# Optimization experiments

Hardware: AMD Instinct MI355X
Metric: run time of the kernel (lower is better)

Reference implementation:

```python
import jax, jax.numpy as jnp
import numpy as np

BAND_WIDTH = 0.05
EPS = 1e-5
NORM_EPS = 1e-12  # F.normalize clamp_min


def _l2_normalize_channels(x):
    # x: (B, C, D, H, W); normalize over channel dim=1 like F.normalize(p=2, dim=1)
    n = jnp.sqrt(jnp.sum(x * x, axis=1, keepdims=True))
    return x / jnp.maximum(n, NORM_EPS)


def setup_inputs() -> dict:
    key = jax.random.key(0)
    k1, k2, k3 = jax.random.split(key, 3)
    B, C, D, H, W = 2, 256, 8, 8, 8
    P, K = 128, 512  # n_patches iterations, k=512 sampled voxels per patch
    S = D * H * W  # 512 spatial voxels
    t2_feat = jax.random.normal(k1, (B, C, D, H, W), dtype=jnp.float32)
    t1_feat = jax.random.normal(k2, (B, C, D, H, W), dtype=jnp.float32)
    idx = jax.random.randint(k3, (P, K), 0, S, dtype=jnp.int32)
    return {"t2_feat": t2_feat, "t1_feat": t1_feat, "idx": idx}


def reference(t2_feat, t1_feat, idx):
    B, C = t2_feat.shape[:2]
    # normalize channels, flatten spatial dims: (B, C, S)
    t2 = _l2_normalize_channels(t2_feat).reshape(B, C, -1)
    t1 = _l2_normalize_channels(t1_feat).reshape(B, C, -1)
    # gather the same random voxels for both modalities: (B, C, P, K)
    t2p = t2[:, :, idx]
    t1p = t1[:, :, idx]
    # batched cosine similarity: bmm(t2p^T, t1p) per patch -> (P, B, K, K)
    cs = jnp.einsum('bcpk,bcpl->pbkl', t2p, t1p)
    e = jnp.exp(cs / BAND_WIDTH)
    pos = jnp.diagonal(e, axis1=2, axis2=3)  # (P, B, K) exp of positives
    # InfoNCE over columns (torch dim=1 of (B,K,K)) and rows (dim=2)
    info_nce1 = pos / jnp.sum(e, axis=2)
    info_nce2 = pos / jnp.sum(e, axis=3)
    info_nce = 0.5 * (info_nce1 + info_nce2)
    # per-patch mean of -log, then mean over patches == global mean
    return jnp.mean(-jnp.log(info_nce + EPS))
```

## Files before the change

### kernel.cpp

```cpp
#include <hip/hip_runtime.h>

typedef __attribute__((ext_vector_type(8))) short bf16x8;
typedef __attribute__((ext_vector_type(4))) float f32x4;

#define C_DIM 256
#define S_DIM 512
#define P_DIM 128
#define K_DIM 512
#define INV_BW 20.0f
#define EPS_LOSS 1e-5f

#define OFF_P2PART 0
#define OFF_P1PART 16384
#define OFF_DIAG   32768
#define OFF_CNTBF  33792
#define OFF_EBF    66560
#define OFF_ETBF   328704
#define OFF_D1P    590848
#define OFF_D2P    852992
#define OFF_PART   1115136
#define OFF_TICKET 1115264

__device__ inline ushort f2bf(float f) {
  union { float f; uint u; } v; v.f = f;
  return (ushort)((v.u + 0x7FFF + ((v.u >> 16) & 1)) >> 16);
}

__global__ __launch_bounds__(512) void pre_kernel(
    const float* __restrict__ t2, const float* __restrict__ t1,
    const int* __restrict__ idx,
    float* __restrict__ p2part, float* __restrict__ p1part,
    ushort* __restrict__ cntbf, int* __restrict__ ticket) {
  int blk = blockIdx.x, t = threadIdx.x;
  if (blk < 32) {
    int b = blk >> 4, g = blk & 15;
    const float* p2 = t2 + b * (C_DIM * S_DIM) + (g * 16) * S_DIM + t;
    const float* p1 = t1 + b * (C_DIM * S_DIM) + (g * 16) * S_DIM + t;
    float a2 = 0.f, a1 = 0.f;
    #pragma unroll
    for (int c = 0; c < 16; ++c) {
      float v2 = p2[c * S_DIM]; a2 += v2 * v2;
      float v1 = p1[c * S_DIM]; a1 += v1 * v1;
    }
    p2part[(b * 16 + g) * S_DIM + t] = a2;
    p1part[(b * 16 + g) * S_DIM + t] = a1;
  } else {
    __shared__ int c_lds[S_DIM];
    int p = blk - 32;
    if (blk == 32 && t == 0) *ticket = 0;
    c_lds[t] = 0;
    __syncthreads();
    atomicAdd(&c_lds[idx[p * K_DIM + t]], 1);
    __syncthreads();
    cntbf[p * S_DIM + t] = f2bf((float)c_lds[t]);
  }
}

__global__ __launch_bounds__(256) void gemm_exp_kernel(
    const float* __restrict__ t2, const float* __restrict__ t1,
    const float* __restrict__ p2part, const float* __restrict__ p1part,
    ushort* __restrict__ Ebf, ushort* __restrict__ ETbf,
    float* __restrict__ diag) {
  __shared__ float At[128][32];
  __shared__ float Bt[128][32];
  __shared__ float As[32], Bs[32];
  int b  = blockIdx.z;
  int s0 = blockIdx.y * 32;
  int t0 = blockIdx.x * 32;
  int tid = threadIdx.x;
  if (tid < 64) {
    int lane = tid & 31;
    const float* src = (tid < 32) ? p2part : p1part;
    int col = ((tid < 32) ? s0 : t0) + lane;
    float ss = 0.f;
    #pragma unroll
    for (int j = 0; j < 16; ++j) ss += src[(b * 16 + j) * S_DIM + col];
    float sc = 1.0f / fmaxf(sqrtf(ss), 1e-12f);
    if (tid < 32) As[lane] = sc; else Bs[lane] = sc;
  }
  __syncthreads();
  int sl = tid & 31, cr = tid >> 5;
  int tx = tid & 15, ty = tid >> 4;
  float ascale = As[sl], bscale = Bs[sl];
  const float* base2 = t2 + b * (C_DIM * S_DIM);
  const float* base1 = t1 + b * (C_DIM * S_DIM);
  float acc00 = 0.f, acc01 = 0.f, acc10 = 0.f, acc11 = 0.f;
  for (int cc = 0; cc < 2; ++cc) {
    int c0 = cc * 128;
    #pragma unroll
    for (int i = 0; i < 16; ++i) {
      int c = cr * 16 + i;
      At[c][sl] = base2[(c0 + c) * S_DIM + s0 + sl] * ascale;
      Bt[c][sl] = base1[(c0 + c) * S_DIM + t0 + sl] * bscale;
    }
    __syncthreads();
    #pragma unroll 8
    for (int c = 0; c < 128; ++c) {
      float2 a  = *reinterpret_cast<const float2*>(&At[c][tx * 2]);
      float2 bv = *reinterpret_cast<const float2*>(&Bt[c][ty * 2]);
      acc00 += a.x * bv.x; acc01 += a.x * bv.y;
      acc10 += a.y * bv.x; acc11 += a.y * bv.y;
    }
    __syncthreads();
  }
  int r0 = s0 + tx * 2, c0o = t0 + ty * 2;
  float e00 = expf(acc00 * INV_BW), e01 = expf(acc01 * INV_BW);
  float e10 = expf(acc10 * INV_BW), e11 = expf(acc11 * INV_BW);
  ushort* Eb  = Ebf  + b * (S_DIM * S_DIM);
  ushort* ETb = ETbf + b * (S_DIM * S_DIM);
  *reinterpret_cast<uint*>(&Eb[r0 * S_DIM + c0o]) =
      (uint)f2bf(e00) | ((uint)f2bf(e01) << 16);
  *reinterpret_cast<uint*>(&Eb[(r0 + 1) * S_DIM + c0o]) =
      (uint)f2bf(e10) | ((uint)f2bf(e11) << 16);
  *reinterpret_cast<uint*>(&ETb[c0o * S_DIM + r0]) =
      (uint)f2bf(e00) | ((uint)f2bf(e10) << 16);
  *reinterpret_cast<uint*>(&ETb[(c0o + 1) * S_DIM + r0]) =
      (uint)f2bf(e01) | ((uint)f2bf(e11) << 16);
  if (blockIdx.x == blockIdx.y && tx == ty) {
    diag[b * S_DIM + r0]     = e00;
    diag[b * S_DIM + r0 + 1] = e11;
  }
}

__global__ __launch_bounds__(256) void denom_mfma_kernel(
    const ushort* __restrict__ Ebf, const ushort* __restrict__ ETbf,
    const ushort* __restrict__ cntbf,
    float* __restrict__ D1p, float* __restrict__ D2p) {
  int wave = threadIdx.x >> 6, lane = threadIdx.x & 63;
  int job = blockIdx.x * 4 + wave;
  int n = job & 31, m = (job >> 5) & 7, b = (job >> 8) & 1;
  int z = (job >> 9) & 1, h = job >> 10;
  int m0 = m * 16, col0 = n * 16;
  const ushort* Bmat = (z ? Ebf : ETbf) + b * (S_DIM * S_DIM);
  float* Dp = (z ? D2p : D1p) + h * (P_DIM * 2 * S_DIM);
  int lr = lane & 15, lo = lane >> 4;
  const ushort* aptr = cntbf + (m0 + lr) * S_DIM + h * 256 + lo * 8;
  const ushort* bptr = Bmat + (col0 + lr) * S_DIM + h * 256 + lo * 8;
  f32x4 acc = {0.f, 0.f, 0.f, 0.f};
  #pragma unroll
  for (int k = 0; k < 8; ++k) {
    bf16x8 af = *reinterpret_cast<const bf16x8*>(aptr + k * 32);
    bf16x8 bfv = *reinterpret_cast<const bf16x8*>(bptr + k * 32);
    acc = __builtin_amdgcn_mfma_f32_16x16x32_bf16(af, bfv, acc, 0, 0, 0);
  }
  #pragma unroll
  for (int r = 0; r < 4; ++r) {
    int p = m0 + lo * 4 + r;
    Dp[(p * 2 + b) * S_DIM + col0 + lr] = acc[r];
  }
}

__global__ __launch_bounds__(512) void loss_final_kernel(
    const int* __restrict__ idx, const float* __restrict__ diag,
    const float* __restrict__ D1p, const float* __restrict__ D2p,
    float* __restrict__ part, int* __restrict__ ticket, float* __restrict__ out) {
  const int HOFF = P_DIM * 2 * S_DIM;
  int p = blockIdx.x, k = threadIdx.x;
  int s = idx[p * K_DIM + k];
  float acc = 0.f;
  #pragma unroll
  for (int b = 0; b < 2; ++b) {
    float pos = diag[b * S_DIM + s];
    int o = (p * 2 + b) * S_DIM + s;
    float d1 = D1p[o] + D1p[HOFF + o];
    float d2 = D2p[o] + D2p[HOFF + o];
    acc += logf(0.5f * (pos / d1 + pos / d2) + EPS_LOSS);
  }
  for (int o = 32; o; o >>= 1) acc += __shfl_down(acc, o);
  __shared__ float red[8];
  __shared__ int lastflag;
  if ((k & 63) == 0) red[k >> 6] = acc;
  __syncthreads();
  if (k == 0) {
    float tsum = 0.f;
    #pragma unroll
    for (int i = 0; i < 8; ++i) tsum += red[i];
    atomicExch(&part[p], tsum);
    __threadfence();
    int old = atomicAdd(ticket, 1);
    lastflag = (old == P_DIM - 1);
  }
  __syncthreads();
  if (lastflag) {
    __threadfence();
    float v = (k < P_DIM) ? atomicAdd(&part[k], 0.0f) : 0.0f;
    for (int o = 32; o; o >>= 1) v += __shfl_down(v, o);
    __shared__ float red2[8];
    if ((k & 63) == 0) red2[k >> 6] = v;
    __syncthreads();
    if (k == 0) {
      float tsum = 0.f;
      #pragma unroll
      for (int i = 0; i < 8; ++i) tsum += red2[i];
      out[0] = -tsum * (1.0f / (P_DIM * 2.0f * K_DIM));
    }
  }
}

extern "C" void kernel_launch(void* const* d_in, const int* in_sizes, int n_in,
                              void* d_out, int out_size, void* d_ws, size_t ws_size,
                              hipStream_t stream) {
  const float* t2 = (const float*)d_in[0];
  const float* t1 = (const float*)d_in[1];
  const int* idx  = (const int*)d_in[2];
  float* ws = (float*)d_ws;
  float*  p2part = ws + OFF_P2PART;
  float*  p1part = ws + OFF_P1PART;
  float*  diag   = ws + OFF_DIAG;
  ushort* cntbf  = (ushort*)(ws + OFF_CNTBF);
  ushort* Ebf    = (ushort*)(ws + OFF_EBF);
  ushort* ETbf   = (ushort*)(ws + OFF_ETBF);
  float*  D1p    = ws + OFF_D1P;
  float*  D2p    = ws + OFF_D2P;
  float*  part   = ws + OFF_PART;
  int*    ticket = (int*)(ws + OFF_TICKET);

  pre_kernel<<<160, 512, 0, stream>>>(t2, t1, idx, p2part, p1part, cntbf, ticket);
  gemm_exp_kernel<<<dim3(16, 16, 2), 256, 0, stream>>>(t2, t1, p2part, p1part,
                                                       Ebf, ETbf, diag);
  denom_mfma_kernel<<<512, 256, 0, stream>>>(Ebf, ETbf, cntbf, D1p, D2p);
  loss_final_kernel<<<P_DIM, 512, 0, stream>>>(idx, diag, D1p, D2p, part, ticket,
                                               (float*)d_out);
}
```

Before: 35.05 us.

## Convert features to transposed bf16 and compute similarity GEMM with MFMA

The pre-kernel now transposes both feature tensors into spatial-major bf16 copies and computes per-voxel full squared norms. The similarity GEMM becomes a bf16 MFMA kernel, one 16x16 tile per wave, with the normalisation scales applied after accumulation. This is meant to replace the fp32 scalar LDS GEMM with matrix-core work. The cost is bf16 rounding of the inputs before the dot product, which scaled by 20 inside exp may lose accuracy. The D1P workspace offset now overlaps the bf16 feature buffers, which is only safe because those are dead by the time denom runs.

```diff
diff --git a/kernel.cpp b/kernel.cpp
--- a/kernel.cpp
+++ b/kernel.cpp
@@ -2,6 +2,7 @@
 
 typedef __attribute__((ext_vector_type(8))) short bf16x8;
 typedef __attribute__((ext_vector_type(4))) float f32x4;
+typedef __attribute__((ext_vector_type(4))) ushort u16x4;
 
 #define C_DIM 256
 #define S_DIM 512
@@ -10,116 +11,115 @@
 #define INV_BW 20.0f
 #define EPS_LOSS 1e-5f
 
-#define OFF_P2PART 0
-#define OFF_P1PART 16384
-#define OFF_DIAG   32768
-#define OFF_CNTBF  33792
-#define OFF_EBF    66560
-#define OFF_ETBF   328704
-#define OFF_D1P    590848
-#define OFF_D2P    852992
-#define OFF_PART   1115136
-#define OFF_TICKET 1115264
+#define OFF_SS2    0
+#define OFF_SS1    1024
+#define OFF_DIAG   2048
+#define OFF_CNTBF  3072
+#define OFF_T2BF   35840
+#define OFF_T1BF   166912
+#define OFF_EBF    297984
+#define OFF_ETBF   560128
+#define OFF_D1P    35840
+#define OFF_D2P    822272
+#define OFF_PART   1084416
+#define OFF_TICKET 1084544
 
 __device__ inline ushort f2bf(float f) {
   union { float f; uint u; } v; v.f = f;
   return (ushort)((v.u + 0x7FFF + ((v.u >> 16) & 1)) >> 16);
 }
 
-__global__ __launch_bounds__(512) void pre_kernel(
+#define TP 260
+__global__ __launch_bounds__(256) void pre_kernel(
     const float* __restrict__ t2, const float* __restrict__ t1,
     const int* __restrict__ idx,
-    float* __restrict__ p2part, float* __restrict__ p1part,
+    float* __restrict__ ss2, float* __restrict__ ss1,
+    ushort* __restrict__ t2bfT, ushort* __restrict__ t1bfT,
     ushort* __restrict__ cntbf, int* __restrict__ ticket) {
-  int blk = blockIdx.x, t = threadIdx.x;
-  if (blk < 32) {
-    int b = blk >> 4, g = blk & 15;
-    const float* p2 = t2 + b * (C_DIM * S_DIM) + (g * 16) * S_DIM + t;
-    const float* p1 = t1 + b * (C_DIM * S_DIM) + (g * 16) * S_DIM + t;
-    float a2 = 0.f, a1 = 0.f;
+  int blk = blockIdx.x, tid = threadIdx.x;
+  if (blk < 64) {
+    __shared__ ushort tl[16][TP];
+    __shared__ float ps[16][17];
+    int b = blk >> 5, stile = blk & 31;
+    int s0 = stile * 16;
+    int ls = tid & 15, cg = tid >> 4;
+    int wv = tid >> 6, ln = tid & 63;
     #pragma unroll
-    for (int c = 0; c < 16; ++c) {
-      float v2 = p2[c * S_DIM]; a2 += v2 * v2;
-      float v1 = p1[c * S_DIM]; a1 += v1 * v1;
+    for (int tt = 0; tt < 2; ++tt) {
+      const float* src = (tt ? t1 : t2) + b * (C_DIM * S_DIM);
+      ushort* dst = (tt ? t1bfT : t2bfT) + b * (S_DIM * C_DIM);
+      float a = 0.f;
+      #pragma unroll
+      for (int k = 0; k < 16; ++k) {
+        int c = cg + 16 * k;
+        float v = src[c * S_DIM + s0 + ls];
+        a += v * v;
+        tl[ls][c] = f2bf(v);
+      }
+      ps[cg][ls] = a;
+      __syncthreads();
+      if (tid < 16) {
+        float ss = 0.f;
+        #pragma unroll
+        for (int j = 0; j < 16; ++j) ss += ps[j][tid];
+        (tt ? ss1 : ss2)[b * S_DIM + s0 + tid] = ss;
+      }
+      #pragma unroll
+      for (int i = 0; i < 4; ++i) {
+        int sl = wv * 4 + i;
+        u16x4 pk = *reinterpret_cast<const u16x4*>(&tl[sl][ln * 4]);
+        *reinterpret_cast<u16x4*>(&dst[(s0 + sl) * C_DIM + ln * 4]) = pk;
+      }
+      __syncthreads();
     }
-    p2part[(b * 16 + g) * S_DIM + t] = a2;
-    p1part[(b * 16 + g) * S_DIM + t] = a1;
   } else {
     __shared__ int c_lds[S_DIM];
-    int p = blk - 32;
-    if (blk == 32 && t == 0) *ticket = 0;
-    c_lds[t] = 0;
+    int p = blk - 64;
+    if (blk == 64 && tid == 0) *ticket = 0;
+    c_lds[tid] = 0; c_lds[tid + 256] = 0;
     __syncthreads();
-    atomicAdd(&c_lds[idx[p * K_DIM + t]], 1);
+    atomicAdd(&c_lds[idx[p * K_DIM + tid]], 1);
+    atomicAdd(&c_lds[idx[p * K_DIM + tid + 256]], 1);
     __syncthreads();
-    cntbf[p * S_DIM + t] = f2bf((float)c_lds[t]);
-  }
-}
-
-__global__ __launch_bounds__(256) void gemm_exp_kernel(
-    const float* __restrict__ t2, const float* __restrict__ t1,
-    const float* __restrict__ p2part, const float* __restrict__ p1part,
+    cntbf[p * S_DIM + tid]       = f2bf((float)c_lds[tid]);
+    cntbf[p * S_DIM + tid + 256] = f2bf((float)c_lds[tid + 256]);
+  }
+}
+
+__global__ __launch_bounds__(256) void gemm_exp_mfma_kernel(
+    const ushort* __restrict__ t2bfT, const ushort* __restrict__ t1bfT,
+    const float* __restrict__ ss2, const float* __restrict__ ss1,
     ushort* __restrict__ Ebf, ushort* __restrict__ ETbf,
     float* __restrict__ diag) {
-  __shared__ float At[128][32];
-  __shared__ float Bt[128][32];
-  __shared__ float As[32], Bs[32];
-  int b  = blockIdx.z;
-  int s0 = blockIdx.y * 32;
-  int t0 = blockIdx.x * 32;
-  int tid = threadIdx.x;
-  if (tid < 64) {
-    int lane = tid & 31;
-    const float* src = (tid < 32) ? p2part : p1part;
-    int col = ((tid < 32) ? s0 : t0) + lane;
-    float ss = 0.f;
-    #pragma unroll
-    for (int j = 0; j < 16; ++j) ss += src[(b * 16 + j) * S_DIM + col];
-    float sc = 1.0f / fmaxf(sqrtf(ss), 1e-12f);
-    if (tid < 32) As[lane] = sc; else Bs[lane] = sc;
-  }
-  __syncthreads();
-  int sl = tid & 31, cr = tid >> 5;
-  int tx = tid & 15, ty = tid >> 4;
-  float ascale = As[sl], bscale = Bs[sl];
-  const float* base2 = t2 + b * (C_DIM * S_DIM);
-  const float* base1 = t1 + b * (C_DIM * S_DIM);
-  float acc00 = 0.f, acc01 = 0.f, acc10 = 0.f, acc11 = 0.f;
-  for (int cc = 0; cc < 2; ++cc) {
-    int c0 = cc * 128;
-    #pragma unroll
-    for (int i = 0; i < 16; ++i) {
-      int c = cr * 16 + i;
-      At[c][sl] = base2[(c0 + c) * S_DIM + s0 + sl] * ascale;
-      Bt[c][sl] = base1[(c0 + c) * S_DIM + t0 + sl] * bscale;
-    }
-    __syncthreads();
-    #pragma unroll 8
-    for (int c = 0; c < 128; ++c) {
-      float2 a  = *reinterpret_cast<const float2*>(&At[c][tx * 2]);
-      float2 bv = *reinterpret_cast<const float2*>(&Bt[c][ty * 2]);
-      acc00 += a.x * bv.x; acc01 += a.x * bv.y;
-      acc10 += a.y * bv.x; acc11 += a.y * bv.y;
-    }
-    __syncthreads();
-  }
-  int r0 = s0 + tx * 2, c0o = t0 + ty * 2;
-  float e00 = expf(acc00 * INV_BW), e01 = expf(acc01 * INV_BW);
-  float e10 = expf(acc10 * INV_BW), e11 = expf(acc11 * INV_BW);
+  int wave = threadIdx.x >> 6, lane = threadIdx.x & 63;
+  int job = blockIdx.x * 4 + wave;
+  int n = job & 31, m = (job >> 5) & 31, b = job >> 10;
+  int m0 = m * 16, c0 = n * 16;
+  int lr = lane & 15, lo = lane >> 4;
+  const ushort* ap = t2bfT + b * (S_DIM * C_DIM) + (m0 + lr) * C_DIM + lo * 8;
+  const ushort* bp = t1bfT + b * (S_DIM * C_DIM) + (c0 + lr) * C_DIM + lo * 8;
+  f32x4 acc = {0.f, 0.f, 0.f, 0.f};
+  #pragma unroll
+  for (int k = 0; k < 8; ++k) {
+    bf16x8 af = *reinterpret_cast<const bf16x8*>(ap + k * 32);
+    bf16x8 bv = *reinterpret_cast<const bf16x8*>(bp + k * 32);
+    acc = __builtin_amdgcn_mfma_f32_16x16x32_bf16(af, bv, acc, 0, 0, 0);
+  }
+  float bs = 1.0f / fmaxf(sqrtf(ss1[b * S_DIM + c0 + lr]), 1e-12f);
+  float e[4]; ushort eb[4];
   ushort* Eb  = Ebf  + b * (S_DIM * S_DIM);
   ushort* ETb = ETbf + b * (S_DIM * S_DIM);
-  *reinterpret_cast<uint*>(&Eb[r0 * S_DIM + c0o]) =
-      (uint)f2bf(e00) | ((uint)f2bf(e01) << 16);
-  *reinterpret_cast<uint*>(&Eb[(r0 + 1) * S_DIM + c0o]) =
-      (uint)f2bf(e10) | ((uint)f2bf(e11) << 16);
-  *reinterpret_cast<uint*>(&ETb[c0o * S_DIM + r0]) =
-      (uint)f2bf(e00) | ((uint)f2bf(e10) << 16);
-  *reinterpret_cast<uint*>(&ETb[(c0o + 1) * S_DIM + r0]) =
-      (uint)f2bf(e01) | ((uint)f2bf(e11) << 16);
-  if (blockIdx.x == blockIdx.y && tx == ty) {
-    diag[b * S_DIM + r0]     = e00;
-    diag[b * S_DIM + r0 + 1] = e11;
-  }
+  #pragma unroll
+  for (int r = 0; r < 4; ++r) {
+    int row = m0 + lo * 4 + r;
+    float as = 1.0f / fmaxf(sqrtf(ss2[b * S_DIM + row]), 1e-12f);
+    e[r] = expf(acc[r] * as * bs * INV_BW);
+    eb[r] = f2bf(e[r]);
+    Eb[row * S_DIM + c0 + lr] = eb[r];
+  }
+  u16x4 pk = {eb[0], eb[1], eb[2], eb[3]};
+  *reinterpret_cast<u16x4*>(&ETb[(c0 + lr) * S_DIM + m0 + lo * 4]) = pk;
+  if (m == n && (lr >> 2) == lo) diag[b * S_DIM + m0 + lr] = e[lr & 3];
 }
 
 __global__ __launch_bounds__(256) void denom_mfma_kernel(
@@ -140,8 +140,8 @@
   #pragma unroll
   for (int k = 0; k < 8; ++k) {
     bf16x8 af = *reinterpret_cast<const bf16x8*>(aptr + k * 32);
-    bf16x8 bfv = *reinterpret_cast<const bf16x8*>(bptr + k * 32);
-    acc = __builtin_amdgcn_mfma_f32_16x16x32_bf16(af, bfv, acc, 0, 0, 0);
+    bf16x8 bv = *reinterpret_cast<const bf16x8*>(bptr + k * 32);
+    acc = __builtin_amdgcn_mfma_f32_16x16x32_bf16(af, bv, acc, 0, 0, 0);
   }
   #pragma unroll
   for (int r = 0; r < 4; ++r) {
@@ -204,10 +204,12 @@
   const float* t1 = (const float*)d_in[1];
   const int* idx  = (const int*)d_in[2];
   float* ws = (float*)d_ws;
-  float*  p2part = ws + OFF_P2PART;
-  float*  p1part = ws + OFF_P1PART;
+  float*  ss2    = ws + OFF_SS2;
+  float*  ss1    = ws + OFF_SS1;
   float*  diag   = ws + OFF_DIAG;
   ushort* cntbf  = (ushort*)(ws + OFF_CNTBF);
+  ushort* t2bfT  = (ushort*)(ws + OFF_T2BF);
+  ushort* t1bfT  = (ushort*)(ws + OFF_T1BF);
   ushort* Ebf    = (ushort*)(ws + OFF_EBF);
   ushort* ETbf   = (ushort*)(ws + OFF_ETBF);
   float*  D1p    = ws + OFF_D1P;
@@ -215,9 +217,10 @@
   float*  part   = ws + OFF_PART;
   int*    ticket = (int*)(ws + OFF_TICKET);
 
-  pre_kernel<<<160, 512, 0, stream>>>(t2, t1, idx, p2part, p1part, cntbf, ticket);
-  gemm_exp_kernel<<<dim3(16, 16, 2), 256, 0, stream>>>(t2, t1, p2part, p1part,
-                                                       Ebf, ETbf, diag);
+  pre_kernel<<<192, 256, 0, stream>>>(t2, t1, idx, ss2, ss1, t2bfT, t1bfT,
+                                      cntbf, ticket);
+  gemm_exp_mfma_kernel<<<512, 256, 0, stream>>>(t2bfT, t1bfT, ss2, ss1,
+                                                Ebf, ETbf, diag);
   denom_mfma_kernel<<<512, 256, 0, stream>>>(Ebf, ETbf, cntbf, D1p, D2p);
   loss_final_kernel<<<P_DIM, 512, 0, stream>>>(idx, diag, D1p, D2p, part, ticket,
                                                (float*)d_out);
```

New measurement: 30.66 us. 12.5% less time.
